# Optimization experiments

Measured on AMD Instinct MI355X. Metric: run time of the kernel, lower is better.

## Reference

```python
import jax, jax.numpy as jnp
import numpy as np

B, S, D, H = 2, 2048, 1024, 16
DK = D // H


def setup_inputs() -> dict:
    key = jax.random.key(0)
    ks = jax.random.split(key, 12)
    s = 1.0 / np.sqrt(D)
    inp = {
        "query": jax.random.normal(ks[0], (B, S, D), jnp.float32),
        "key_": jax.random.normal(ks[1], (B, S, D), jnp.float32),
        "value": jax.random.normal(ks[2], (B, S, D), jnp.float32),
        # causal mask, broadcast over heads: [B, 1, S, S]
        "mask": jnp.broadcast_to(jnp.tril(jnp.ones((S, S), bool)), (B, 1, S, S)),
        "W_q": jax.random.uniform(ks[3], (D, D), jnp.float32, -s, s),
        "b_q": jax.random.uniform(ks[4], (D,), jnp.float32, -s, s),
        "W_k": jax.random.uniform(ks[5], (D, D), jnp.float32, -s, s),
        "b_k": jax.random.uniform(ks[6], (D,), jnp.float32, -s, s),
        "W_v": jax.random.uniform(ks[7], (D, D), jnp.float32, -s, s),
        "b_v": jax.random.uniform(ks[8], (D,), jnp.float32, -s, s),
        "W_o": jax.random.uniform(ks[9], (D, D), jnp.float32, -s, s),
        "b_o": jax.random.uniform(ks[10], (D,), jnp.float32, -s, s),
    }
    return inp


def reference(query, key_, value, mask, W_q, b_q, W_k, b_k, W_v, b_v, W_o, b_o):
    b = query.shape[0]
    # linear projections (torch Linear: x @ W.T + b)
    Q = query @ W_q.T + b_q
    K = key_ @ W_k.T + b_k
    V = value @ W_v.T + b_v
    # [b, S, H, dk] -> [b, H, S, dk]
    Q = Q.reshape(b, -1, H, DK).transpose(0, 2, 1, 3)
    K = K.reshape(b, -1, H, DK).transpose(0, 2, 1, 3)
    V = V.reshape(b, -1, H, DK).transpose(0, 2, 1, 3)
    scores = jnp.einsum("bhqd,bhkd->bhqk", Q, K) / jnp.sqrt(jnp.float32(DK))
    scores = jnp.where(mask, scores, -jnp.inf)
    attn = jax.nn.softmax(scores, axis=-1)
    out = jnp.einsum("bhqk,bhkd->bhqd", attn, V)
    out = out.transpose(0, 2, 1, 3).reshape(b, -1, D)
    return out @ W_o.T + b_o
```

## Files before the change

### kernel.cpp

```cpp
#include <hip/hip_runtime.h>
#include <hip/hip_bf16.h>
#include <stdint.h>

#define B_ 2
#define S_ 2048
#define D_ 1024
#define H_ 16
#define DK_ 64

typedef __attribute__((ext_vector_type(4))) float floatx4;
typedef __attribute__((ext_vector_type(8))) short shortx8;
typedef __attribute__((ext_vector_type(4))) short shortx4;
typedef unsigned short ushort_t;

__device__ inline ushort_t f2bf(float f) {
  union { float f; unsigned u; } v; v.f = f;
  unsigned r = v.u + 0x7FFFu + ((v.u >> 16) & 1u);
  return (ushort_t)(r >> 16);
}

__device__ inline unsigned pack2bf(float lo, float hi) {
  return __builtin_amdgcn_perm(__float_as_uint(hi), __float_as_uint(lo), 0x07060302u);
}

__device__ inline shortx4 mk_sx4(unsigned lo, unsigned hi) {
  union { unsigned u[2]; shortx4 s; } v; v.u[0] = lo; v.u[1] = hi; return v.s;
}

__device__ inline float fast_exp2(float x) {
#if __has_builtin(__builtin_amdgcn_exp2f)
  return __builtin_amdgcn_exp2f(x);
#else
  return __expf(0.69314718056f * x);
#endif
}

__device__ inline void gload_lds16(const void* g, void* l) {
  __builtin_amdgcn_global_load_lds(
      (const __attribute__((address_space(1))) unsigned int*)g,
      (__attribute__((address_space(3))) unsigned int*)l, 16, 0, 0);
}

__device__ inline floatx4 mfma16x16x16bf16(shortx4 a, shortx4 b, floatx4 c) {
#if __has_builtin(__builtin_amdgcn_mfma_f32_16x16x16bf16_1k)
  return __builtin_amdgcn_mfma_f32_16x16x16bf16_1k(a, b, c, 0, 0, 0);
#else
  floatx4 d;
  asm("v_mfma_f32_16x16x16_bf16 %0, %1, %2, %3" : "=v"(d) : "v"(a), "v"(b), "v"(c));
  return d;
#endif
}

struct ConvArgs {
  const float* src[7];
  ushort_t* dst[7];
};

__global__ __launch_bounds__(256) void convert_kernel(ConvArgs a) {
  int blk = blockIdx.x;
  int seg, bis;
  if (blk < 3072) { seg = blk >> 10; bis = blk & 1023; }
  else { int bb = blk - 3072; seg = 3 + (bb >> 8); bis = bb & 255; }
  const float4* src = (const float4*)(a.src[seg]) + (size_t)bis * 1024;
  ushort4* dst = (ushort4*)(a.dst[seg]) + (size_t)bis * 1024;
#pragma unroll
  for (int i = 0; i < 4; ++i) {
    int idx = i * 256 + threadIdx.x;
    float4 v = src[idx];
    ushort4 o;
    o.x = f2bf(v.x); o.y = f2bf(v.y); o.z = f2bf(v.z); o.w = f2bf(v.w);
    dst[idx] = o;
  }
}

template <int TM>
__device__ inline void gemm_bk64_core(const ushort_t* __restrict__ A,
                                      const ushort_t* __restrict__ W,
                                      const float* __restrict__ bias,
                                      float scl,
                                      void* __restrict__ outp,
                                      int m0, int n0, int N, int K, int outmode) {
  constexpr int GA = TM / 8;
  constexpr int GB = 16;
  constexpr int GW = (GA + GB) / 4;
  constexpr int MI = TM / 32;
  constexpr int BUFB = (TM + 128) * 128;
  __shared__ uint4 smem4[2 * BUFB / 16];
  char* smem = (char*)&smem4[0];

  const int tid = threadIdx.x;
  const int wave = tid >> 6;
  const int lane = tid & 63;
  const int quad = lane >> 4;
  const int l16 = lane & 15;
  const int wm = (wave >> 1) * (TM / 2);
  const int wn = (wave & 1) * 64;

  floatx4 acc[MI][4] = {};

  const ushort_t* gsrc[GW];
  int ldst[GW];
#pragma unroll
  for (int i = 0; i < GW; ++i) {
    int g = wave * GW + i;
    int r8 = lane >> 3;
    int cs = ((lane & 7) ^ r8) * 8;
    if (g < GA) {
      gsrc[i] = A + (size_t)(m0 + g * 8 + r8) * K + cs;
      ldst[i] = g * 1024 + lane * 16;
    } else {
      gsrc[i] = W + (size_t)(n0 + (g - GA) * 8 + r8) * K + cs;
      ldst[i] = TM * 128 + (g - GA) * 1024 + lane * 16;
    }
  }

#pragma unroll
  for (int i = 0; i < GW; ++i) gload_lds16(gsrc[i], smem + ldst[i]);

  const int niter = K >> 6;
  for (int j = 0; j < niter; ++j) {
    __syncthreads();
    if (j + 1 < niter) {
      const int ko = (j + 1) * 64;
      char* bufn = smem + ((j + 1) & 1) * BUFB;
#pragma unroll
      for (int i = 0; i < GW; ++i) gload_lds16(gsrc[i] + ko, bufn + ldst[i]);
    }
    const char* aT = smem + (j & 1) * BUFB;
    const char* bT = aT + TM * 128;
    shortx8 af[MI][2], bf[4][2];
#pragma unroll
    for (int ks = 0; ks < 2; ++ks) {
      const int co = ((ks * 4 + quad) ^ (l16 & 7)) * 16;
#pragma unroll
      for (int mi = 0; mi < MI; ++mi)
        af[mi][ks] = *(const shortx8*)(aT + (wm + mi * 16 + l16) * 128 + co);
#pragma unroll
      for (int ni = 0; ni < 4; ++ni)
        bf[ni][ks] = *(const shortx8*)(bT + (wn + ni * 16 + l16) * 128 + co);
    }
#pragma unroll
    for (int ks = 0; ks < 2; ++ks)
#pragma unroll
      for (int mi = 0; mi < MI; ++mi)
#pragma unroll
        for (int ni = 0; ni < 4; ++ni)
          acc[mi][ni] = __builtin_amdgcn_mfma_f32_16x16x32_bf16(af[mi][ks], bf[ni][ks], acc[mi][ni], 0, 0, 0);
  }

#pragma unroll
  for (int ni = 0; ni < 4; ++ni) {
    int n = n0 + wn + ni * 16 + l16;
    float bv = bias[n];
#pragma unroll
    for (int mi = 0; mi < MI; ++mi) {
      if (outmode == 2) {
        int m = m0 + wm + mi * 16 + quad * 4;
        int b = m >> 11, s = m & 2047;
        ushort_t* dst = (ushort_t*)outp + (((size_t)(b * 1024 + n)) << 11) + s;
        uint2 pk;
        pk.x = (unsigned)f2bf(acc[mi][ni][0] + bv) |
               ((unsigned)f2bf(acc[mi][ni][1] + bv) << 16);
        pk.y = (unsigned)f2bf(acc[mi][ni][2] + bv) |
               ((unsigned)f2bf(acc[mi][ni][3] + bv) << 16);
        *(uint2*)(dst) = pk;
      } else {
#pragma unroll
        for (int r = 0; r < 4; ++r) {
          int m = m0 + wm + mi * 16 + quad * 4 + r;
          float v = (acc[mi][ni][r] + bv) * scl;
          if (outmode == 1) ((float*)outp)[(size_t)m * N + n] = v;
          else ((ushort_t*)outp)[(size_t)m * N + n] = f2bf(v);
        }
      }
    }
  }
}

struct QkvArgs {
  const ushort_t* A[3];
  const ushort_t* W[3];
  const float* bias[3];
  ushort_t* out[3];
  float scale[3];
};

__global__ __launch_bounds__(256) void gemm_qkv_kernel(QkvArgs a) {
  int z = blockIdx.z;
  int m0 = (blockIdx.x * 4 + (blockIdx.y >> 3)) * 128;
  int n0 = (blockIdx.y & 7) * 128;
  gemm_bk64_core<128>(a.A[z], a.W[z], a.bias[z], a.scale[z], a.out[z],
                      m0, n0, D_, D_, z == 2 ? 2 : 0);
}

__global__ __launch_bounds__(256) void gemm_out_kernel(const ushort_t* __restrict__ A,
                                                       const ushort_t* __restrict__ W,
                                                       const float* __restrict__ bias,
                                                       float* __restrict__ out) {
  int m0 = (blockIdx.x * 8 + (blockIdx.y >> 3)) * 64;
  int n0 = (blockIdx.y & 7) * 128;
  gemm_bk64_core<64>(A, W, bias, 1.0f, out, m0, n0, D_, D_, 1);
}

__global__ __launch_bounds__(256, 2) void attn_kernel(const ushort_t* __restrict__ Qp,
                                                      const ushort_t* __restrict__ Kp,
                                                      const ushort_t* __restrict__ Vt,
                                                      ushort_t* __restrict__ O) {
  const int id = blockIdx.x;
  const int h = id & 15;
  const int qq = (id & 255) >> 4;
  const int b = id >> 8;
  const int qt = b ? qq : 15 - qq;
  const int q0 = qt * 128;
  const int tid = threadIdx.x;
  const int wave = tid >> 6;
  const int lane = tid & 63;
  const int quad = lane >> 4;
  const int l16 = lane & 15;

  __shared__ ushort_t smem[2][16384];

  const size_t hoff = (size_t)h * DK_;

  shortx8 qf[2][2];
#pragma unroll
  for (int grp = 0; grp < 2; ++grp) {
    const ushort_t* qrow = Qp + ((size_t)b * S_ + q0 + wave * 32 + grp * 16 + l16) * D_ + hoff;
#pragma unroll
    for (int ks = 0; ks < 2; ++ks)
      qf[grp][ks] = *(const shortx8*)(qrow + ks * 32 + quad * 8);
  }

  const int r8 = lane >> 3;
  const int jj8 = ((lane & 7) ^ r8) * 8;
  const ushort_t* kb[4];
#pragma unroll
  for (int g = 0; g < 4; ++g) {
    int r = wave * 32 + g * 8 + r8;
    kb[g] = Kp + ((size_t)b * S_ + r) * D_ + hoff + jj8;
  }
  const int r4 = lane >> 4;
  const ushort_t* vb[4];
#pragma unroll
  for (int g = 0; g < 4; ++g) {
    int r = wave * 16 + g * 4 + r4;
    int cpos = ((lane & 15) ^ ((g * 4 + r4) & 15)) * 8;
    vb[g] = Vt + ((size_t)(b * H_ + h) * 64 + r) * S_ + cpos;
  }

  floatx4 oacc[2][4] = {};
  float l_run[2] = {0.f, 0.f};
  const int nj = qt + 1;
  const int qwave_max = q0 + wave * 32 + 31;

#pragma unroll
  for (int g = 0; g < 4; ++g) {
    gload_lds16(kb[g], &smem[0][wave * 2048 + g * 512]);
    gload_lds16(vb[g], &smem[0][8192 + wave * 2048 + g * 512]);
  }

  for (int j = 0; j < nj; ++j) {
    __syncthreads();
    if (j + 1 < nj) {
      ushort_t* bufn = smem[(j + 1) & 1];
      const size_t ko = (size_t)(j + 1) * 128 * D_;
      const int vo = (j + 1) * 128;
#pragma unroll
      for (int g = 0; g < 4; ++g) {
        gload_lds16(kb[g] + ko, bufn + wave * 2048 + g * 512);
        gload_lds16(vb[g] + vo, bufn + 8192 + wave * 2048 + g * 512);
      }
    }
    if (j * 128 > qwave_max) continue;
    const ushort_t* k_lds = smem[j & 1];
    const ushort_t* v_lds = smem[j & 1] + 8192;

#pragma unroll
    for (int half = 0; half < 2; ++half) {
      const int kbase = j * 128 + half * 64;
      if (kbase > qwave_max) break;

      floatx4 sacc[2][4];
      __builtin_amdgcn_s_setprio(1);
#pragma unroll
      for (int kkb = 0; kkb < 4; ++kkb) {
        const ushort_t* krow = k_lds + (half * 64 + kkb * 16 + l16) * 64;
        shortx8 af0 = *(const shortx8*)(krow + (quad ^ (l16 & 7)) * 8);
        shortx8 af1 = *(const shortx8*)(krow + ((4 | quad) ^ (l16 & 7)) * 8);
#pragma unroll
        for (int grp = 0; grp < 2; ++grp) {
          floatx4 acc = {0.f, 0.f, 0.f, 0.f};
          acc = __builtin_amdgcn_mfma_f32_16x16x32_bf16(af0, qf[grp][0], acc, 0, 0, 0);
          acc = __builtin_amdgcn_mfma_f32_16x16x32_bf16(af1, qf[grp][1], acc, 0, 0, 0);
          sacc[grp][kkb] = acc;
        }
      }
      __builtin_amdgcn_s_setprio(0);
#pragma unroll
      for (int grp = 0; grp < 2; ++grp) {
        const int qg = q0 + wave * 32 + grp * 16 + l16;
        if (kbase + 63 > q0 + wave * 32 + grp * 16) {
#pragma unroll
          for (int kkb = 0; kkb < 4; ++kkb)
#pragma unroll
            for (int r = 0; r < 4; ++r)
              if (kbase + kkb * 16 + quad * 4 + r > qg) sacc[grp][kkb][r] = -3.0e38f;
        }
      }

      shortx4 pf[2][4];
#pragma unroll
      for (int grp = 0; grp < 2; ++grp) {
        float psum = 0.f;
#pragma unroll
        for (int kkb = 0; kkb < 4; ++kkb) {
          float p0 = fast_exp2(sacc[grp][kkb][0]);
          float p1 = fast_exp2(sacc[grp][kkb][1]);
          float p2 = fast_exp2(sacc[grp][kkb][2]);
          float p3 = fast_exp2(sacc[grp][kkb][3]);
          psum += (p0 + p1) + (p2 + p3);
          pf[grp][kkb] = mk_sx4(pack2bf(p0, p1), pack2bf(p2, p3));
        }
        l_run[grp] += psum;
      }

      __builtin_amdgcn_s_setprio(1);
#pragma unroll
      for (int kkb = 0; kkb < 4; ++kkb) {
        const int jj = ((half * 8 + kkb * 2 + (quad >> 1)) ^ l16) * 8 + (quad & 1) * 4;
#pragma unroll
        for (int db = 0; db < 4; ++db) {
          shortx4 vf = *(const shortx4*)(v_lds + (db * 16 + l16) * 128 + jj);
          oacc[0][db] = mfma16x16x16bf16(vf, pf[0][kkb], oacc[0][db]);
          oacc[1][db] = mfma16x16x16bf16(vf, pf[1][kkb], oacc[1][db]);
        }
      }
      __builtin_amdgcn_s_setprio(0);
    }
  }

  __syncthreads();
  ushort_t* sm = &smem[0][0];
#pragma unroll
  for (int grp = 0; grp < 2; ++grp) {
    float l0 = l_run[grp];
    l0 += __shfl_xor(l0, 16);
    l0 += __shfl_xor(l0, 32);
    float inv_l = 1.0f / l0;
    int row = wave * 32 + grp * 16 + l16;
#pragma unroll
    for (int db = 0; db < 4; ++db) {
#pragma unroll
      for (int rr = 0; rr < 2; ++rr) {
        unsigned pk = pack2bf(oacc[grp][db][rr * 2] * inv_l, oacc[grp][db][rr * 2 + 1] * inv_l);
        *(unsigned*)(sm + row * 72 + db * 16 + quad * 4 + rr * 2) = pk;
      }
    }
  }
  __syncthreads();
  {
    int r = tid >> 1, c = (tid & 1) * 32;
    const ushort_t* src = sm + r * 72 + c;
    ushort_t* dst = O + ((size_t)b * S_ + q0 + r) * D_ + hoff + c;
    uint4 v0 = *(const uint4*)(src);
    uint4 v1 = *(const uint4*)(src + 8);
    uint4 v2 = *(const uint4*)(src + 16);
    uint4 v3 = *(const uint4*)(src + 24);
    *(uint4*)(dst) = v0;
    *(uint4*)(dst + 8) = v1;
    *(uint4*)(dst + 16) = v2;
    *(uint4*)(dst + 24) = v3;
  }
}

extern "C" void kernel_launch(void* const* d_in, const int* in_sizes, int n_in,
                              void* d_out, int out_size, void* d_ws, size_t ws_size,
                              hipStream_t stream) {
  (void)in_sizes; (void)n_in; (void)out_size; (void)ws_size;
  char* ws = (char*)d_ws;
  ushort_t* xq = (ushort_t*)(ws + 0);
  ushort_t* xk = (ushort_t*)(ws + 8388608);
  ushort_t* xv = (ushort_t*)(ws + 16777216);
  ushort_t* wq = (ushort_t*)(ws + 25165824);
  ushort_t* wk = (ushort_t*)(ws + 27262976);
  ushort_t* wv = (ushort_t*)(ws + 29360128);
  ushort_t* wo = (ushort_t*)(ws + 31457280);
  ushort_t* Qp = (ushort_t*)(ws + 33554432);
  ushort_t* Kp = (ushort_t*)(ws + 41943040);
  ushort_t* Vt = (ushort_t*)(ws + 50331648);
  ushort_t* O = xq;

  ConvArgs ca;
  ca.src[0] = (const float*)d_in[0];  ca.dst[0] = xq;
  ca.src[1] = (const float*)d_in[1];  ca.dst[1] = xk;
  ca.src[2] = (const float*)d_in[2];  ca.dst[2] = xv;
  ca.src[3] = (const float*)d_in[4];  ca.dst[3] = wq;
  ca.src[4] = (const float*)d_in[6];  ca.dst[4] = wk;
  ca.src[5] = (const float*)d_in[8];  ca.dst[5] = wv;
  ca.src[6] = (const float*)d_in[10]; ca.dst[6] = wo;
  convert_kernel<<<dim3(4096), dim3(256), 0, stream>>>(ca);

  QkvArgs qa;
  qa.A[0] = xq; qa.W[0] = wq; qa.bias[0] = (const float*)d_in[5]; qa.out[0] = Qp;
  qa.A[1] = xk; qa.W[1] = wk; qa.bias[1] = (const float*)d_in[7]; qa.out[1] = Kp;
  qa.A[2] = xv; qa.W[2] = wv; qa.bias[2] = (const float*)d_in[9]; qa.out[2] = Vt;
  qa.scale[0] = 0.125f * 1.44269504089f;
  qa.scale[1] = 1.0f;
  qa.scale[2] = 1.0f;
  gemm_qkv_kernel<<<dim3(8, 32, 3), dim3(256), 0, stream>>>(qa);

  attn_kernel<<<dim3(512), dim3(256), 0, stream>>>(Qp, Kp, Vt, O);

  gemm_out_kernel<<<dim3(8, 64, 1), dim3(256), 0, stream>>>(
      O, wo, (const float*)d_in[11], (float*)d_out);
}
```

Before: 233.2 us.

## Shrink attention query tile to 64 rows and double grid for occupancy

The attention kernel now processes 64 query rows per block (one 16-row group per wave) with 64-key tiles, instead of 128 rows and 128-key tiles. The grid doubles to 1024 blocks, shared memory halves, and launch bounds request 4 blocks per CU, all aimed at better load balance across the causal triangle and more latency hiding. The cost is less K/V reuse per block, so more global/LDS traffic and more barriers per unit of work. The LDS swizzle for V is reworked to match the smaller tile.

```diff
diff --git a/kernel.cpp b/kernel.cpp
--- a/kernel.cpp
+++ b/kernel.cpp
@@ -202,174 +202,150 @@
   gemm_bk64_core<64>(A, W, bias, 1.0f, out, m0, n0, D_, D_, 1);
 }
 
-__global__ __launch_bounds__(256, 2) void attn_kernel(const ushort_t* __restrict__ Qp,
+__global__ __launch_bounds__(256, 4) void attn_kernel(const ushort_t* __restrict__ Qp,
                                                       const ushort_t* __restrict__ Kp,
                                                       const ushort_t* __restrict__ Vt,
                                                       ushort_t* __restrict__ O) {
   const int id = blockIdx.x;
   const int h = id & 15;
-  const int qq = (id & 255) >> 4;
-  const int b = id >> 8;
-  const int qt = b ? qq : 15 - qq;
-  const int q0 = qt * 128;
+  const int u = (id >> 4) & 31;
+  const int b = id >> 9;
+  const int qt = b ? u : 31 - u;
+  const int q0 = qt * 64;
   const int tid = threadIdx.x;
   const int wave = tid >> 6;
   const int lane = tid & 63;
   const int quad = lane >> 4;
   const int l16 = lane & 15;
 
-  __shared__ ushort_t smem[2][16384];
+  __shared__ ushort_t smem[2][8192];
 
   const size_t hoff = (size_t)h * DK_;
 
-  shortx8 qf[2][2];
-#pragma unroll
-  for (int grp = 0; grp < 2; ++grp) {
-    const ushort_t* qrow = Qp + ((size_t)b * S_ + q0 + wave * 32 + grp * 16 + l16) * D_ + hoff;
-#pragma unroll
-    for (int ks = 0; ks < 2; ++ks)
-      qf[grp][ks] = *(const shortx8*)(qrow + ks * 32 + quad * 8);
+  shortx8 qf[2];
+  {
+    const ushort_t* qrow = Qp + ((size_t)b * S_ + q0 + wave * 16 + l16) * D_ + hoff;
+    qf[0] = *(const shortx8*)(qrow + quad * 8);
+    qf[1] = *(const shortx8*)(qrow + 32 + quad * 8);
   }
 
   const int r8 = lane >> 3;
-  const int jj8 = ((lane & 7) ^ r8) * 8;
-  const ushort_t* kb[4];
-#pragma unroll
-  for (int g = 0; g < 4; ++g) {
-    int r = wave * 32 + g * 8 + r8;
-    kb[g] = Kp + ((size_t)b * S_ + r) * D_ + hoff + jj8;
-  }
-  const int r4 = lane >> 4;
-  const ushort_t* vb[4];
-#pragma unroll
-  for (int g = 0; g < 4; ++g) {
-    int r = wave * 16 + g * 4 + r4;
-    int cpos = ((lane & 15) ^ ((g * 4 + r4) & 15)) * 8;
-    vb[g] = Vt + ((size_t)(b * H_ + h) * 64 + r) * S_ + cpos;
-  }
-
-  floatx4 oacc[2][4] = {};
-  float l_run[2] = {0.f, 0.f};
+  const int cs8 = ((lane & 7) ^ r8) * 8;
+  const ushort_t* kb[2];
+  const ushort_t* vb[2];
+  int kdst[2], vdst[2];
+#pragma unroll
+  for (int g = 0; g < 2; ++g) {
+    const int tr = wave * 16 + g * 8 + r8;
+    kb[g] = Kp + ((size_t)b * S_ + tr) * D_ + hoff + cs8;
+    vb[g] = Vt + ((size_t)(b * H_ + h) * 64 + tr) * (size_t)S_ + cs8;
+    kdst[g] = (wave * 16 + g * 8) * 64 + lane * 8;
+    vdst[g] = 4096 + (wave * 16 + g * 8) * 64 + lane * 8;
+  }
+
+  floatx4 oacc[4] = {};
+  float l_run = 0.f;
   const int nj = qt + 1;
-  const int qwave_max = q0 + wave * 32 + 31;
-
-#pragma unroll
-  for (int g = 0; g < 4; ++g) {
-    gload_lds16(kb[g], &smem[0][wave * 2048 + g * 512]);
-    gload_lds16(vb[g], &smem[0][8192 + wave * 2048 + g * 512]);
+
+#pragma unroll
+  for (int g = 0; g < 2; ++g) {
+    gload_lds16(kb[g], &smem[0][kdst[g]]);
+    gload_lds16(vb[g], &smem[0][vdst[g]]);
   }
 
   for (int j = 0; j < nj; ++j) {
     __syncthreads();
     if (j + 1 < nj) {
       ushort_t* bufn = smem[(j + 1) & 1];
-      const size_t ko = (size_t)(j + 1) * 128 * D_;
-      const int vo = (j + 1) * 128;
-#pragma unroll
-      for (int g = 0; g < 4; ++g) {
-        gload_lds16(kb[g] + ko, bufn + wave * 2048 + g * 512);
-        gload_lds16(vb[g] + vo, bufn + 8192 + wave * 2048 + g * 512);
-      }
-    }
-    if (j * 128 > qwave_max) continue;
+      const size_t ko = (size_t)(j + 1) * 64 * D_;
+      const int vo = (j + 1) * 64;
+#pragma unroll
+      for (int g = 0; g < 2; ++g) {
+        gload_lds16(kb[g] + ko, bufn + kdst[g]);
+        gload_lds16(vb[g] + vo, bufn + vdst[g]);
+      }
+    }
     const ushort_t* k_lds = smem[j & 1];
-    const ushort_t* v_lds = smem[j & 1] + 8192;
-
-#pragma unroll
-    for (int half = 0; half < 2; ++half) {
-      const int kbase = j * 128 + half * 64;
-      if (kbase > qwave_max) break;
-
-      floatx4 sacc[2][4];
-      __builtin_amdgcn_s_setprio(1);
+    const ushort_t* v_lds = smem[j & 1] + 4096;
+
+    floatx4 sacc[4];
+    __builtin_amdgcn_s_setprio(1);
+#pragma unroll
+    for (int kkb = 0; kkb < 4; ++kkb) {
+      const ushort_t* krow = k_lds + (kkb * 16 + l16) * 64;
+      shortx8 af0 = *(const shortx8*)(krow + (quad ^ (l16 & 7)) * 8);
+      shortx8 af1 = *(const shortx8*)(krow + ((4 | quad) ^ (l16 & 7)) * 8);
+      floatx4 acc = {0.f, 0.f, 0.f, 0.f};
+      acc = __builtin_amdgcn_mfma_f32_16x16x32_bf16(af0, qf[0], acc, 0, 0, 0);
+      acc = __builtin_amdgcn_mfma_f32_16x16x32_bf16(af1, qf[1], acc, 0, 0, 0);
+      sacc[kkb] = acc;
+    }
+    __builtin_amdgcn_s_setprio(0);
+
+    const int kbase = j * 64;
+    if (kbase + 63 > q0 + wave * 16) {
+      const int qg = q0 + wave * 16 + l16;
+#pragma unroll
+      for (int kkb = 0; kkb < 4; ++kkb)
+#pragma unroll
+        for (int r = 0; r < 4; ++r)
+          if (kbase + kkb * 16 + quad * 4 + r > qg) sacc[kkb][r] = -3.0e38f;
+    }
+
+    shortx4 pf[4];
+    {
+      float psum = 0.f;
 #pragma unroll
       for (int kkb = 0; kkb < 4; ++kkb) {
-        const ushort_t* krow = k_lds + (half * 64 + kkb * 16 + l16) * 64;
-        shortx8 af0 = *(const shortx8*)(krow + (quad ^ (l16 & 7)) * 8);
-        shortx8 af1 = *(const shortx8*)(krow + ((4 | quad) ^ (l16 & 7)) * 8);
-#pragma unroll
-        for (int grp = 0; grp < 2; ++grp) {
-          floatx4 acc = {0.f, 0.f, 0.f, 0.f};
-          acc = __builtin_amdgcn_mfma_f32_16x16x32_bf16(af0, qf[grp][0], acc, 0, 0, 0);
-          acc = __builtin_amdgcn_mfma_f32_16x16x32_bf16(af1, qf[grp][1], acc, 0, 0, 0);
-          sacc[grp][kkb] = acc;
-        }
-      }
-      __builtin_amdgcn_s_setprio(0);
-#pragma unroll
-      for (int grp = 0; grp < 2; ++grp) {
-        const int qg = q0 + wave * 32 + grp * 16 + l16;
-        if (kbase + 63 > q0 + wave * 32 + grp * 16) {
-#pragma unroll
-          for (int kkb = 0; kkb < 4; ++kkb)
-#pragma unroll
-            for (int r = 0; r < 4; ++r)
-              if (kbase + kkb * 16 + quad * 4 + r > qg) sacc[grp][kkb][r] = -3.0e38f;
-        }
-      }
-
-      shortx4 pf[2][4];
-#pragma unroll
-      for (int grp = 0; grp < 2; ++grp) {
-        float psum = 0.f;
-#pragma unroll
-        for (int kkb = 0; kkb < 4; ++kkb) {
-          float p0 = fast_exp2(sacc[grp][kkb][0]);
-          float p1 = fast_exp2(sacc[grp][kkb][1]);
-          float p2 = fast_exp2(sacc[grp][kkb][2]);
-          float p3 = fast_exp2(sacc[grp][kkb][3]);
-          psum += (p0 + p1) + (p2 + p3);
-          pf[grp][kkb] = mk_sx4(pack2bf(p0, p1), pack2bf(p2, p3));
-        }
-        l_run[grp] += psum;
-      }
-
-      __builtin_amdgcn_s_setprio(1);
-#pragma unroll
-      for (int kkb = 0; kkb < 4; ++kkb) {
-        const int jj = ((half * 8 + kkb * 2 + (quad >> 1)) ^ l16) * 8 + (quad & 1) * 4;
-#pragma unroll
-        for (int db = 0; db < 4; ++db) {
-          shortx4 vf = *(const shortx4*)(v_lds + (db * 16 + l16) * 128 + jj);
-          oacc[0][db] = mfma16x16x16bf16(vf, pf[0][kkb], oacc[0][db]);
-          oacc[1][db] = mfma16x16x16bf16(vf, pf[1][kkb], oacc[1][db]);
-        }
-      }
-      __builtin_amdgcn_s_setprio(0);
-    }
+        float p0 = fast_exp2(sacc[kkb][0]);
+        float p1 = fast_exp2(sacc[kkb][1]);
+        float p2 = fast_exp2(sacc[kkb][2]);
+        float p3 = fast_exp2(sacc[kkb][3]);
+        psum += (p0 + p1) + (p2 + p3);
+        pf[kkb] = mk_sx4(pack2bf(p0, p1), pack2bf(p2, p3));
+      }
+      l_run += psum;
+    }
+
+    __builtin_amdgcn_s_setprio(1);
+#pragma unroll
+    for (int kkb = 0; kkb < 4; ++kkb) {
+      const int jj = ((kkb * 2 + (quad >> 1)) ^ (l16 & 7)) * 8 + (quad & 1) * 4;
+#pragma unroll
+      for (int db = 0; db < 4; ++db) {
+        shortx4 vf = *(const shortx4*)(v_lds + (db * 16 + l16) * 64 + jj);
+        oacc[db] = mfma16x16x16bf16(vf, pf[kkb], oacc[db]);
+      }
+    }
+    __builtin_amdgcn_s_setprio(0);
   }
 
   __syncthreads();
   ushort_t* sm = &smem[0][0];
-#pragma unroll
-  for (int grp = 0; grp < 2; ++grp) {
-    float l0 = l_run[grp];
+  {
+    float l0 = l_run;
     l0 += __shfl_xor(l0, 16);
     l0 += __shfl_xor(l0, 32);
     float inv_l = 1.0f / l0;
-    int row = wave * 32 + grp * 16 + l16;
+    int row = wave * 16 + l16;
 #pragma unroll
     for (int db = 0; db < 4; ++db) {
 #pragma unroll
       for (int rr = 0; rr < 2; ++rr) {
-        unsigned pk = pack2bf(oacc[grp][db][rr * 2] * inv_l, oacc[grp][db][rr * 2 + 1] * inv_l);
+        unsigned pk = pack2bf(oacc[db][rr * 2] * inv_l, oacc[db][rr * 2 + 1] * inv_l);
         *(unsigned*)(sm + row * 72 + db * 16 + quad * 4 + rr * 2) = pk;
       }
     }
   }
   __syncthreads();
   {
-    int r = tid >> 1, c = (tid & 1) * 32;
+    int r = tid >> 2, c = (tid & 3) * 16;
     const ushort_t* src = sm + r * 72 + c;
     ushort_t* dst = O + ((size_t)b * S_ + q0 + r) * D_ + hoff + c;
     uint4 v0 = *(const uint4*)(src);
     uint4 v1 = *(const uint4*)(src + 8);
-    uint4 v2 = *(const uint4*)(src + 16);
-    uint4 v3 = *(const uint4*)(src + 24);
     *(uint4*)(dst) = v0;
     *(uint4*)(dst + 8) = v1;
-    *(uint4*)(dst + 16) = v2;
-    *(uint4*)(dst + 24) = v3;
   }
 }
 
@@ -409,7 +385,7 @@
   qa.scale[2] = 1.0f;
   gemm_qkv_kernel<<<dim3(8, 32, 3), dim3(256), 0, stream>>>(qa);
 
-  attn_kernel<<<dim3(512), dim3(256), 0, stream>>>(Qp, Kp, Vt, O);
+  attn_kernel<<<dim3(1024), dim3(256), 0, stream>>>(Qp, Kp, Vt, O);
 
   gemm_out_kernel<<<dim3(8, 64, 1), dim3(256), 0, stream>>>(
       O, wo, (const float*)d_in[11], (float*)d_out);
```

New measurement: 223.9 us. 1.04x faster.
